# Kernel tuning notes

Hardware: AMD Instinct MI355X
Metric: run time of the kernel (lower is better)

Reference implementation:

```python
import jax, jax.numpy as jnp
import numpy as np

# BasicLS (deep_gnss): batched weighted least squares x_hat = pinv(W A) (W r)
# with W = diag(ones) == identity, so WA == A and Wr == r mathematically.
# A = [-los_x, -los_y, -los_z, 1] per measurement, r = pseudorange residual.

B = 262144  # batch of GNSS epochs
M = 32      # satellite measurements per epoch
DIM = 4     # [residual, los_x, los_y, los_z]


def setup_inputs() -> dict:
    key = jax.random.key(0)
    kx, _ = jax.random.split(key)
    x = jax.random.normal(kx, (B, M, DIM), dtype=jnp.float32)
    pad_mask = jnp.zeros((B, M), dtype=bool)  # unused by the module's forward
    return {"x": x, "pad_mask": pad_mask}


def reference(x, pad_mask):
    Bb, Mm, _ = x.shape
    # A: [B, M, 4] = concat(-x[:,:,1:4], ones)
    A = jnp.concatenate([-x[:, :, 1:4], jnp.ones((Bb, Mm, 1), dtype=x.dtype)], axis=-1)
    r = x[:, :, 0:1]  # [B, M, 1]
    # W = diag_embed(ones) is the identity, so WA = A and Wr = r.
    A_pinv = jnp.linalg.pinv(A)          # [B, 4, M] (SVD-based, matches torch.pinverse)
    out = jnp.matmul(A_pinv, r)[..., 0]  # [B, 4]
    return out
```

## Files before the change

kernel.cpp:

```cpp
#include <hip/hip_runtime.h>


__global__ __launch_bounds__(256) void basicls_kernel(const float* __restrict__ x,
                                                      float* __restrict__ out,
                                                      int B) {
    int b = blockIdx.x * blockDim.x + threadIdx.x;
    if (b >= B) return;

    const float4* __restrict__ xb = reinterpret_cast<const float4*>(x) + (size_t)b * 32;

    float s11 = 0.f, s12 = 0.f, s13 = 0.f, s22 = 0.f, s23 = 0.f, s33 = 0.f;
    float s1 = 0.f, s2 = 0.f, s3 = 0.f;
    float t1 = 0.f, t2 = 0.f, t3 = 0.f, t0 = 0.f;

#pragma unroll
    for (int m = 0; m < 32; ++m) {
        float4 v = xb[m];
        float r  = v.x;
        float a1 = v.y, a2 = v.z, a3 = v.w;
        s11 = fmaf(a1, a1, s11);
        s12 = fmaf(a1, a2, s12);
        s13 = fmaf(a1, a3, s13);
        s22 = fmaf(a2, a2, s22);
        s23 = fmaf(a2, a3, s23);
        s33 = fmaf(a3, a3, s33);
        s1 += a1; s2 += a2; s3 += a3;
        t1 = fmaf(a1, r, t1);
        t2 = fmaf(a2, r, t2);
        t3 = fmaf(a3, r, t3);
        t0 += r;
    }

    float G[4][4];
    G[0][0] = s11; G[0][1] = s12; G[0][2] = s13; G[0][3] = -s1;
    G[1][0] = s12; G[1][1] = s22; G[1][2] = s23; G[1][3] = -s2;
    G[2][0] = s13; G[2][1] = s23; G[2][2] = s33; G[2][3] = -s3;
    G[3][0] = -s1; G[3][1] = -s2; G[3][2] = -s3; G[3][3] = 32.0f;
    float rhs[4] = { -t1, -t2, -t3, t0 };

    float L[4][4];
#pragma unroll
    for (int k = 0; k < 4; ++k) {
        float d = G[k][k];
#pragma unroll
        for (int j = 0; j < 4; ++j) {
            if (j < k) d = fmaf(-L[k][j], L[k][j], d);
        }
        float lkk = sqrtf(fmaxf(d, 1e-30f));
        L[k][k] = lkk;
        float inv = __frcp_rn(lkk);
#pragma unroll
        for (int i = 0; i < 4; ++i) {
            if (i > k) {
                float s = G[i][k];
#pragma unroll
                for (int j = 0; j < 4; ++j) {
                    if (j < k) s = fmaf(-L[i][j], L[k][j], s);
                }
                L[i][k] = s * inv;
            }
        }
    }

    float y[4];
#pragma unroll
    for (int i = 0; i < 4; ++i) {
        float s = rhs[i];
#pragma unroll
        for (int j = 0; j < 4; ++j) {
            if (j < i) s = fmaf(-L[i][j], y[j], s);
        }
        y[i] = s * __frcp_rn(L[i][i]);
    }

    float w[4];
#pragma unroll
    for (int i = 3; i >= 0; --i) {
        float s = y[i];
#pragma unroll
        for (int j = 0; j < 4; ++j) {
            if (j > i) s = fmaf(-L[j][i], w[j], s);
        }
        w[i] = s * __frcp_rn(L[i][i]);
    }

    float4 wv = make_float4(w[0], w[1], w[2], w[3]);
    reinterpret_cast<float4*>(out)[b] = wv;
}

extern "C" void kernel_launch(void* const* d_in, const int* in_sizes, int n_in,
                              void* d_out, int out_size, void* d_ws, size_t ws_size,
                              hipStream_t stream) {
    const float* x = (const float*)d_in[0];
    float* out = (float*)d_out;
    int B = in_sizes[0] / (32 * 4);
    dim3 block(256);
    dim3 grid((B + 255) / 256);
    basicls_kernel<<<grid, block, 0, stream>>>(x, out, B);
}
```

Before: 204.1 us.

## Stage batch tiles into LDS via async global_load_lds with coalesced loads

Replaces per-thread strided float4 loads, where each thread reads its own 512-byte row, with coalesced block-wide async global-to-LDS copies of a 64-epoch tile. Threads then read their rows from LDS using a rotated index so that lanes hit different banks. The block size drops to 64 and the bounds check is removed, so the code assumes B is a multiple of 64. The 32 KB of LDS per block may limit how many blocks fit on each CU.

```diff
diff --git a/kernel.cpp b/kernel.cpp
--- a/kernel.cpp
+++ b/kernel.cpp
@@ -1,21 +1,37 @@
 #include <hip/hip_runtime.h>
 
 
-__global__ __launch_bounds__(256) void basicls_kernel(const float* __restrict__ x,
-                                                      float* __restrict__ out,
-                                                      int B) {
-    int b = blockIdx.x * blockDim.x + threadIdx.x;
-    if (b >= B) return;
+#define GLOBAL_AS __attribute__((address_space(1)))
+#define LDS_AS    __attribute__((address_space(3)))
 
-    const float4* __restrict__ xb = reinterpret_cast<const float4*>(x) + (size_t)b * 32;
+__device__ __forceinline__ void async_copy16(const float4* gptr, float4* lptr) {
+    __builtin_amdgcn_global_load_lds((const GLOBAL_AS void*)gptr,
+                                     (LDS_AS void*)lptr, 16, 0, 0);
+}
 
+__global__ __launch_bounds__(64) void basicls_kernel(const float* __restrict__ x,
+                                                     float* __restrict__ out) {
+    __shared__ float4 tile[64 * 32];
+
+    const int t  = threadIdx.x;
+    const int b0 = blockIdx.x * 64;
+
+    const float4* src = reinterpret_cast<const float4*>(x) + (size_t)b0 * 32;
+#pragma unroll
+    for (int k = 0; k < 32; ++k) {
+        async_copy16(src + k * 64 + t, tile + k * 64);
+    }
+    __syncthreads();
+
+    const int base = t * 32;
     float s11 = 0.f, s12 = 0.f, s13 = 0.f, s22 = 0.f, s23 = 0.f, s33 = 0.f;
     float s1 = 0.f, s2 = 0.f, s3 = 0.f;
     float t1 = 0.f, t2 = 0.f, t3 = 0.f, t0 = 0.f;
 
 #pragma unroll
     for (int m = 0; m < 32; ++m) {
-        float4 v = xb[m];
+        int idx = base + ((m + t) & 31);
+        float4 v = tile[idx];
         float r  = v.x;
         float a1 = v.y, a2 = v.z, a3 = v.w;
         s11 = fmaf(a1, a1, s11);
@@ -84,8 +100,7 @@
         w[i] = s * __frcp_rn(L[i][i]);
     }
 
-    float4 wv = make_float4(w[0], w[1], w[2], w[3]);
-    reinterpret_cast<float4*>(out)[b] = wv;
+    reinterpret_cast<float4*>(out)[b0 + t] = make_float4(w[0], w[1], w[2], w[3]);
 }
 
 extern "C" void kernel_launch(void* const* d_in, const int* in_sizes, int n_in,
@@ -94,7 +109,7 @@
     const float* x = (const float*)d_in[0];
     float* out = (float*)d_out;
     int B = in_sizes[0] / (32 * 4);
-    dim3 block(256);
-    dim3 grid((B + 255) / 256);
-    basicls_kernel<<<grid, block, 0, stream>>>(x, out, B);
+    dim3 block(64);
+    dim3 grid(B / 64);
+    basicls_kernel<<<grid, block, 0, stream>>>(x, out);
 }
```

Result: no change. 201.2 us (-1.4%).
